# Performance work log

Hardware: AMD Instinct MI355X
Metric: run time of the kernel (lower is better)

The kernel has to match this reference:

```python
import jax, jax.numpy as jnp
import numpy as np

B, T, F, S, H, A = 32768, 64, 64, 5, 128, 16  # batch, obs_len, fut_len, state, hidden, adapter


def _gru_cell(x, h, Wih, Whh, bih, bhh):
    # PyTorch GRUCell math: gates ordered (r, z, n)
    gx = x @ Wih.T + bih
    gh = h @ Whh.T + bhh
    rx, zx, nx = jnp.split(gx, 3, axis=-1)
    rh, zh, nh = jnp.split(gh, 3, axis=-1)
    r = jax.nn.sigmoid(rx + rh)
    z = jax.nn.sigmoid(zx + zh)
    n = jnp.tanh(nx + r * nh)
    return (1.0 - z) * n + z * h


def setup_inputs() -> dict:
    key = jax.random.key(0)
    ks = jax.random.split(key, 24)
    p = lambda k, shp: jax.random.normal(k, shp, jnp.float32) * 0.05
    return {
        "obs": jax.random.normal(ks[0], (B, T, S), jnp.float32),
        "target": jax.random.normal(ks[1], (B, F, S), jnp.float32),
        "dataset_ids": jax.random.randint(ks[2], (B,), 0, 4),
        "enc_Wih": p(ks[3], (3 * H, S)), "enc_Whh": p(ks[4], (3 * H, H)),
        "enc_bih": p(ks[5], (3 * H,)), "enc_bhh": p(ks[6], (3 * H,)),
        "cell_Wih": p(ks[7], (3 * H, S)), "cell_Whh": p(ks[8], (3 * H, H)),
        "cell_bih": p(ks[9], (3 * H,)), "cell_bhh": p(ks[10], (3 * H,)),
        "head_W": p(ks[11], (S, H)), "head_b": p(ks[12], (S,)),
        "pp_W1": p(ks[13], (A, H)), "pp_b1": p(ks[14], (A,)),
        "pp_W2": p(ks[15], (H, A)), "pp_b2": p(ks[16], (H,)),
        "pk_W1": p(ks[17], (A, H)), "pk_b1": p(ks[18], (A,)),
        "pk_W2": p(ks[19], (H, A)), "pk_b2": p(ks[20], (H,)),
    }


def reference(obs, target, dataset_ids,
              enc_Wih, enc_Whh, enc_bih, enc_bhh,
              cell_Wih, cell_Whh, cell_bih, cell_bhh,
              head_W, head_b,
              pp_W1, pp_b1, pp_W2, pp_b2,
              pk_W1, pk_b1, pk_W2, pk_b2):
    b = obs.shape[0]
    # Encoder GRU over obs -> final hidden state [B, H]
    h0 = jnp.zeros((b, H), obs.dtype)
    def enc_step(h, x):
        return _gru_cell(x, h, enc_Wih, enc_Whh, enc_bih, enc_bhh), None
    h_t, _ = jax.lax.scan(enc_step, h0, jnp.swapaxes(obs, 0, 1))

    pm = (dataset_ids == 0)[:, None]  # pointodyssey routed to private_point
    km = (dataset_ids == 1)[:, None]  # kubric routed to private_kubric

    def adapt(h):
        dp = jax.nn.relu(h @ pp_W1.T + pp_b1) @ pp_W2.T + pp_b2
        dk = jax.nn.relu(h @ pk_W1.T + pk_b1) @ pk_W2.T + pk_b2
        return h + jnp.where(pm, dp, 0.0) + jnp.where(km, dk, 0.0)

    # Teacher-forced inputs: x_0 = obs[:, -1], x_t = target[:, t-1]
    xs = jnp.concatenate([obs[:, -1:, :], target[:, :-1, :]], axis=1)  # [B, F, S]
    def roll_step(h, x):
        h = _gru_cell(x, h, cell_Wih, cell_Whh, cell_bih, cell_bhh)
        h = adapt(h)
        return h, h @ head_W.T + head_b
    _, preds = jax.lax.scan(roll_step, h_t, jnp.swapaxes(xs, 0, 1))  # [F, B, S]
    return jnp.swapaxes(preds, 0, 1)  # [B, F, S]
```

## Files before the change

kernel.cpp:

```cpp
#include <hip/hip_runtime.h>

#define B_TOT 32768
#define T_OBS 64
#define F_FUT 64
#define S_DIM 5
#define H_DIM 128
#define A_DIM 16
#define R_BLK 64
#define NTHREADS 512
#define XSTR 320
#define HPAD 132
#define XPAD 36
#define APAD 24

typedef __attribute__((ext_vector_type(8))) short short8;
typedef __attribute__((ext_vector_type(4))) float f32x4;

union U8 { short8 v; unsigned int u[4]; unsigned short s[8]; };

__device__ __forceinline__ unsigned short f2bf(float f) {
  unsigned int u = __float_as_uint(f);
  u += 0x7FFFu + ((u >> 16) & 1u);
  return (unsigned short)(u >> 16);
}

__device__ __forceinline__ f32x4 MFMA(short8 a, short8 b, f32x4 c) {
  return __builtin_amdgcn_mfma_f32_16x16x32_bf16(a, b, c, 0, 0, 0);
}

__device__ __forceinline__ float sigm(float x) {
  return __builtin_amdgcn_rcpf(1.0f + __expf(-x));
}
__device__ __forceinline__ float tanh_(float x) {
  return 2.0f * __builtin_amdgcn_rcpf(1.0f + __expf(-2.0f * x)) - 1.0f;
}

__device__ __forceinline__ short8 load_w(const float* __restrict__ W, int ld,
                                         int g0, int gmax, int kmax, int ks,
                                         int lr, int lg) {
  U8 a;
  const int g = g0 + lr;
  #pragma unroll
  for (int i = 0; i < 8; ++i) {
    int k = 32 * ks + 16 * (i >> 2) + 4 * lg + (i & 3);
    float v = (g < gmax && k < kmax) ? W[g * ld + k] : 0.0f;
    a.s[i] = f2bf(v);
  }
  return a.v;
}

__device__ __forceinline__ void ld_bfrag(U8& b, const unsigned short* p) {
  uint2 t0 = *(const uint2*)p;
  uint2 t1 = *(const uint2*)(p + 16);
  b.u[0] = t0.x; b.u[1] = t0.y; b.u[2] = t1.x; b.u[3] = t1.y;
}

__device__ __forceinline__ void gru_step(
    const unsigned short* __restrict__ hb, const unsigned short* __restrict__ xb,
    const short8 (&fh)[3][4], const short8 (&fx)[3],
    const f32x4& brz0, const f32x4& brz1, const f32x4& bnh, const f32x4& bnx,
    const float (&h_old)[4][4], float (&hn)[4][4], int lr, int lg)
{
  f32x4 aR[4], aZ[4], aN[4], aX[4];
  #pragma unroll
  for (int rt = 0; rt < 4; ++rt) {
    const unsigned short* hp = hb + (rt * 16 + lr) * HPAD + 4 * lg;
    const unsigned short* xp = xb + (rt * 16 + lr) * XPAD + 4 * lg;
    U8 bx;
    { uint2 t = *(const uint2*)xp; bx.u[0] = t.x; bx.u[1] = t.y; bx.u[2] = 0u; bx.u[3] = 0u; }
    U8 bh0; ld_bfrag(bh0, hp);
    aR[rt] = MFMA(fh[0][0], bh0.v, brz0);
    aZ[rt] = MFMA(fh[1][0], bh0.v, brz1);
    aN[rt] = MFMA(fh[2][0], bh0.v, bnh);
    #pragma unroll
    for (int ks = 1; ks < 4; ++ks) {
      U8 bh; ld_bfrag(bh, hp + 32 * ks);
      aR[rt] = MFMA(fh[0][ks], bh.v, aR[rt]);
      aZ[rt] = MFMA(fh[1][ks], bh.v, aZ[rt]);
      aN[rt] = MFMA(fh[2][ks], bh.v, aN[rt]);
    }
    aR[rt] = MFMA(fx[0], bx.v, aR[rt]);
    aZ[rt] = MFMA(fx[1], bx.v, aZ[rt]);
    aX[rt] = MFMA(fx[2], bx.v, bnx);
  }
  #pragma unroll
  for (int rt = 0; rt < 4; ++rt) {
    #pragma unroll
    for (int i = 0; i < 4; ++i) {
      float r = sigm(aR[rt][i]);
      float z = sigm(aZ[rt][i]);
      float n = tanh_(aX[rt][i] + r * aN[rt][i]);
      hn[rt][i] = z * (h_old[rt][i] - n) + n;
    }
  }
}

__device__ __forceinline__ void write_h(unsigned short* hd, const float (&v)[4][4],
                                        int w, int lr, int lg) {
  #pragma unroll
  for (int rt = 0; rt < 4; ++rt) {
    uint2 t;
    t.x = (unsigned)f2bf(v[rt][0]) | ((unsigned)f2bf(v[rt][1]) << 16);
    t.y = (unsigned)f2bf(v[rt][2]) | ((unsigned)f2bf(v[rt][3]) << 16);
    *(uint2*)(hd + (rt * 16 + lr) * HPAD + 16 * w + 4 * lg) = t;
  }
}

__global__ __launch_bounds__(NTHREADS, 2) void trace_gru_kernel(
    const float* __restrict__ obs, const float* __restrict__ target,
    const int* __restrict__ ids,
    const float* __restrict__ eWih, const float* __restrict__ eWhh,
    const float* __restrict__ ebih, const float* __restrict__ ebhh,
    const float* __restrict__ cWih, const float* __restrict__ cWhh,
    const float* __restrict__ cbih, const float* __restrict__ cbhh,
    const float* __restrict__ headW, const float* __restrict__ headb,
    const float* __restrict__ ppW1, const float* __restrict__ ppb1,
    const float* __restrict__ ppW2, const float* __restrict__ ppb2,
    const float* __restrict__ pkW1, const float* __restrict__ pkb1,
    const float* __restrict__ pkW2, const float* __restrict__ pkb2,
    float* __restrict__ out)
{
  __shared__ __align__(16) unsigned short h_lds[2][R_BLK * HPAD];
  __shared__ __align__(16) unsigned short x_lds[2][R_BLK * XPAD];
  __shared__ __align__(16) unsigned short a_lds[2 * R_BLK * APAD];
  __shared__ __align__(16) unsigned short wd_lds[12 * 64 * 8];

  const int tid = threadIdx.x;
  const int lane = tid & 63;
  const int w = tid >> 6;
  const int lr = lane & 15;
  const int lg = lane >> 4;
  const int row0 = blockIdx.x * R_BLK;

  {
    unsigned int* p = (unsigned int*)&h_lds[0][0];
    for (int i = tid; i < R_BLK * HPAD / 2; i += NTHREADS) p[i] = 0u;
    unsigned int* q = (unsigned int*)&x_lds[0][0];
    for (int i = tid; i < 2 * R_BLK * XPAD / 2; i += NTHREADS) q[i] = 0u;
  }
  __syncthreads();

  const int sx_row = tid / 5;
  const int sx_s = tid - 5 * sx_row;
  if (tid < 320)
    x_lds[0][sx_row * XPAD + sx_s] = f2bf(obs[(row0 + sx_row) * XSTR + sx_s]);

  float pmf[4], kmf[4];
  #pragma unroll
  for (int rt = 0; rt < 4; ++rt) {
    int id = ids[row0 + rt * 16 + lr];
    pmf[rt] = (id == 0) ? 1.0f : 0.0f;
    kmf[rt] = (id == 1) ? 1.0f : 0.0f;
  }

  short8 fh[3][4], fx[3];
  f32x4 brz0, brz1, bnh, bnx;
  #pragma unroll
  for (int mt = 0; mt < 3; ++mt) {
    #pragma unroll
    for (int ks = 0; ks < 4; ++ks)
      fh[mt][ks] = load_w(eWhh, H_DIM, mt * H_DIM + 16 * w, 384, H_DIM, ks, lr, lg);
    fx[mt] = load_w(eWih, S_DIM, mt * H_DIM + 16 * w, 384, S_DIM, 0, lr, lg);
  }
  #pragma unroll
  for (int i = 0; i < 4; ++i) {
    int g = 16 * w + 4 * lg + i;
    brz0[i] = ebih[g] + ebhh[g];
    brz1[i] = ebih[H_DIM + g] + ebhh[H_DIM + g];
    bnh[i]  = ebhh[2 * H_DIM + g];
    bnx[i]  = ebih[2 * H_DIM + g];
  }

  float h_reg[4][4];
  #pragma unroll
  for (int rt = 0; rt < 4; ++rt)
    #pragma unroll
    for (int i = 0; i < 4; ++i) h_reg[rt][i] = 0.0f;

  __syncthreads();

  for (int u = 0; u < T_OBS; ++u) {
    float hn[4][4];
    gru_step(h_lds[u & 1], x_lds[u & 1], fh, fx, brz0, brz1, bnh, bnx, h_reg, hn, lr, lg);
    #pragma unroll
    for (int rt = 0; rt < 4; ++rt)
      #pragma unroll
      for (int i = 0; i < 4; ++i) h_reg[rt][i] = hn[rt][i];
    write_h(h_lds[(u + 1) & 1], h_reg, w, lr, lg);
    if (tid < 320) {
      int un = u + 1;
      int tsrc = (un < T_OBS) ? un : (T_OBS - 1);
      x_lds[un & 1][sx_row * XPAD + sx_s] =
          f2bf(obs[(row0 + sx_row) * XSTR + tsrc * S_DIM + sx_s]);
    }
    __syncthreads();
  }

  #pragma unroll
  for (int mt = 0; mt < 3; ++mt) {
    #pragma unroll
    for (int ks = 0; ks < 4; ++ks)
      fh[mt][ks] = load_w(cWhh, H_DIM, mt * H_DIM + 16 * w, 384, H_DIM, ks, lr, lg);
    fx[mt] = load_w(cWih, S_DIM, mt * H_DIM + 16 * w, 384, S_DIM, 0, lr, lg);
  }
  #pragma unroll
  for (int i = 0; i < 4; ++i) {
    int g = 16 * w + 4 * lg + i;
    brz0[i] = cbih[g] + cbhh[g];
    brz1[i] = cbih[H_DIM + g] + cbhh[H_DIM + g];
    bnh[i]  = cbhh[2 * H_DIM + g];
    bnx[i]  = cbih[2 * H_DIM + g];
  }
  short8 fW2[2];
  fW2[0] = load_w(ppW2, A_DIM, 16 * w, H_DIM, A_DIM, 0, lr, lg);
  fW2[1] = load_w(pkW2, A_DIM, 16 * w, H_DIM, A_DIM, 0, lr, lg);
  f32x4 b1v, b2v0, b2v1, hbv;
  {
    const float* b1p = (w & 1) ? pkb1 : ppb1;
    #pragma unroll
    for (int i = 0; i < 4; ++i) {
      b1v[i]  = b1p[4 * lg + i];
      b2v0[i] = ppb2[16 * w + 4 * lg + i];
      b2v1[i] = pkb2[16 * w + 4 * lg + i];
      int s = 4 * lg + i;
      hbv[i] = (s < S_DIM) ? headb[s] : 0.0f;
    }
  }
  for (int f = w; f < 12; f += 8) {
    short8 v;
    if (f < 8) {
      const float* W1 = (f >> 2) ? pkW1 : ppW1;
      v = load_w(W1, H_DIM, 0, A_DIM, H_DIM, f & 3, lr, lg);
    } else {
      v = load_w(headW, H_DIM, 0, S_DIM, H_DIM, f - 8, lr, lg);
    }
    *(short8*)&wd_lds[(f * 64 + lane) * 8] = v;
  }
  __syncthreads();

  for (int d = 0; d < F_FUT; ++d) {
    const int u = T_OBS + d;
    float hn[4][4];
    gru_step(h_lds[0], x_lds[u & 1], fh, fx, brz0, brz1, bnh, bnx, h_reg, hn, lr, lg);
    write_h(h_lds[1], hn, w, lr, lg);
    __syncthreads();

    {
      const int aa = w & 1, art = w >> 1;
      const unsigned short* hp = &h_lds[1][(art * 16 + lr) * HPAD + 4 * lg];
      U8 bh0; ld_bfrag(bh0, hp);
      f32x4 acc = MFMA(*(const short8*)&wd_lds[((aa * 4 + 0) * 64 + lane) * 8], bh0.v, b1v);
      #pragma unroll
      for (int ks = 1; ks < 4; ++ks) {
        U8 bh; ld_bfrag(bh, hp + 32 * ks);
        acc = MFMA(*(const short8*)&wd_lds[((aa * 4 + ks) * 64 + lane) * 8], bh.v, acc);
      }
      uint2 t;
      t.x = (unsigned)f2bf(fmaxf(acc[0], 0.f)) | ((unsigned)f2bf(fmaxf(acc[1], 0.f)) << 16);
      t.y = (unsigned)f2bf(fmaxf(acc[2], 0.f)) | ((unsigned)f2bf(fmaxf(acc[3], 0.f)) << 16);
      *(uint2*)&a_lds[(aa * R_BLK + art * 16 + lr) * APAD + 4 * lg] = t;
    }
    __syncthreads();

    #pragma unroll
    for (int rt = 0; rt < 4; ++rt) {
      U8 b0, b1_;
      { uint2 t = *(const uint2*)&a_lds[(0 * R_BLK + rt * 16 + lr) * APAD + 4 * lg];
        b0.u[0] = t.x; b0.u[1] = t.y; b0.u[2] = 0u; b0.u[3] = 0u; }
      { uint2 t = *(const uint2*)&a_lds[(1 * R_BLK + rt * 16 + lr) * APAD + 4 * lg];
        b1_.u[0] = t.x; b1_.u[1] = t.y; b1_.u[2] = 0u; b1_.u[3] = 0u; }
      f32x4 d0 = MFMA(fW2[0], b0.v, b2v0);
      f32x4 d1 = MFMA(fW2[1], b1_.v, b2v1);
      #pragma unroll
      for (int i = 0; i < 4; ++i)
        h_reg[rt][i] = hn[rt][i] + pmf[rt] * d0[i] + kmf[rt] * d1[i];
    }
    write_h(h_lds[0], h_reg, w, lr, lg);
    if (d < F_FUT - 1 && tid < 320) {
      int un = u + 1;
      x_lds[un & 1][sx_row * XPAD + sx_s] =
          f2bf(target[(row0 + sx_row) * XSTR + (un - T_OBS - 1) * S_DIM + sx_s]);
    }
    __syncthreads();

    if (w < 4) {
      const unsigned short* hp = &h_lds[0][(w * 16 + lr) * HPAD + 4 * lg];
      U8 bh0; ld_bfrag(bh0, hp);
      f32x4 acc = MFMA(*(const short8*)&wd_lds[((8 + 0) * 64 + lane) * 8], bh0.v, hbv);
      #pragma unroll
      for (int ks = 1; ks < 4; ++ks) {
        U8 bh; ld_bfrag(bh, hp + 32 * ks);
        acc = MFMA(*(const short8*)&wd_lds[((8 + ks) * 64 + lane) * 8], bh.v, acc);
      }
      float* op = out + (size_t)((row0 + w * 16 + lr) * F_FUT + d) * S_DIM;
      if (lg == 0) { op[0] = acc[0]; op[1] = acc[1]; op[2] = acc[2]; op[3] = acc[3]; }
      else if (lg == 1) { op[4] = acc[0]; }
    }
  }
}

extern "C" void kernel_launch(void* const* d_in, const int* in_sizes, int n_in,
                              void* d_out, int out_size, void* d_ws, size_t ws_size,
                              hipStream_t stream) {
  (void)in_sizes; (void)n_in; (void)out_size; (void)d_ws; (void)ws_size;
  const float* obs    = (const float*)d_in[0];
  const float* target = (const float*)d_in[1];
  const int*   ids    = (const int*)d_in[2];
  const float* eWih = (const float*)d_in[3];
  const float* eWhh = (const float*)d_in[4];
  const float* ebih = (const float*)d_in[5];
  const float* ebhh = (const float*)d_in[6];
  const float* cWih = (const float*)d_in[7];
  const float* cWhh = (const float*)d_in[8];
  const float* cbih = (const float*)d_in[9];
  const float* cbhh = (const float*)d_in[10];
  const float* headW = (const float*)d_in[11];
  const float* headb = (const float*)d_in[12];
  const float* ppW1 = (const float*)d_in[13];
  const float* ppb1 = (const float*)d_in[14];
  const float* ppW2 = (const float*)d_in[15];
  const float* ppb2 = (const float*)d_in[16];
  const float* pkW1 = (const float*)d_in[17];
  const float* pkb1 = (const float*)d_in[18];
  const float* pkW2 = (const float*)d_in[19];
  const float* pkb2 = (const float*)d_in[20];

  dim3 grid(B_TOT / R_BLK), block(NTHREADS);
  trace_gru_kernel<<<grid, block, 0, stream>>>(
      obs, target, ids,
      eWih, eWhh, ebih, ebhh,
      cWih, cWhh, cbih, cbhh,
      headW, headb,
      ppW1, ppb1, ppW2, ppb2,
      pkW1, pkb1, pkW2, pkb2,
      (float*)d_out);
}
```

Measured before the change: 793.4 us.

## Swizzle hidden-state LDS layout, prescale gate weights, prefetch inputs, fuse GRU epilogue

Replaces the padded hidden-state LDS layout with an XOR-style swizzled 128-wide layout. This allows single 16-byte reads per MFMA B fragment instead of two 8-byte reads. Gate weights and biases are prescaled by log2(e) so activations use exp2 directly, and bf16 packing uses the hardware v_cvt_pk_bf16_f32 instruction. Per-row-tile state writes are fused into the GRU step, and next-step inputs are prefetched from global memory a step ahead to hide load latency. The risks are bf16 rounding of prescaled weights and higher register pressure from the prefetch.

```diff
diff --git a/kernel.cpp b/kernel.cpp
--- a/kernel.cpp
+++ b/kernel.cpp
@@ -9,14 +9,23 @@
 #define R_BLK 64
 #define NTHREADS 512
 #define XSTR 320
-#define HPAD 132
+#define HSTR 128
 #define XPAD 36
 #define APAD 24
 
+#define LOG2E 1.4426950408889634f
+#define L2E2  2.8853900817779268f
+
 typedef __attribute__((ext_vector_type(8))) short short8;
 typedef __attribute__((ext_vector_type(4))) float f32x4;
 
 union U8 { short8 v; unsigned int u[4]; unsigned short s[8]; };
+
+#if __has_builtin(__builtin_amdgcn_exp2f)
+#define EXP2(x) __builtin_amdgcn_exp2f(x)
+#else
+#define EXP2(x) exp2f(x)
+#endif
 
 __device__ __forceinline__ unsigned short f2bf(float f) {
   unsigned int u = __float_as_uint(f);
@@ -24,85 +33,91 @@
   return (unsigned short)(u >> 16);
 }
 
+__device__ __forceinline__ unsigned cvtpk(float a, float b) {
+  unsigned r;
+  asm("v_cvt_pk_bf16_f32 %0, %1, %2" : "=v"(r) : "v"(a), "v"(b));
+  return r;
+}
+
 __device__ __forceinline__ f32x4 MFMA(short8 a, short8 b, f32x4 c) {
   return __builtin_amdgcn_mfma_f32_16x16x32_bf16(a, b, c, 0, 0, 0);
 }
 
-__device__ __forceinline__ float sigm(float x) {
-  return __builtin_amdgcn_rcpf(1.0f + __expf(-x));
-}
-__device__ __forceinline__ float tanh_(float x) {
-  return 2.0f * __builtin_amdgcn_rcpf(1.0f + __expf(-2.0f * x)) - 1.0f;
+__device__ __forceinline__ short8 h_read(const unsigned short* base, int row, int ks, int lg) {
+  return *(const short8*)(base + row * HSTR + (((4 * ks + lg + row) & 15) << 3));
+}
+__device__ __forceinline__ void h_write(unsigned short* base, int row, int w, int lg,
+                                        unsigned lo, unsigned hi) {
+  unsigned short* p = base + row * HSTR +
+                      (((4 * (w >> 1) + lg + row) & 15) << 3) + ((w & 1) << 2);
+  *(uint2*)p = make_uint2(lo, hi);
 }
 
 __device__ __forceinline__ short8 load_w(const float* __restrict__ W, int ld,
                                          int g0, int gmax, int kmax, int ks,
-                                         int lr, int lg) {
+                                         int lr, int lg, float scale) {
   U8 a;
   const int g = g0 + lr;
   #pragma unroll
   for (int i = 0; i < 8; ++i) {
     int k = 32 * ks + 16 * (i >> 2) + 4 * lg + (i & 3);
-    float v = (g < gmax && k < kmax) ? W[g * ld + k] : 0.0f;
+    float v = (g < gmax && k < kmax) ? W[g * ld + k] * scale : 0.0f;
     a.s[i] = f2bf(v);
   }
   return a.v;
 }
 
-__device__ __forceinline__ void ld_bfrag(U8& b, const unsigned short* p) {
-  uint2 t0 = *(const uint2*)p;
-  uint2 t1 = *(const uint2*)(p + 16);
-  b.u[0] = t0.x; b.u[1] = t0.y; b.u[2] = t1.x; b.u[3] = t1.y;
+__device__ __forceinline__ float xload(const float* __restrict__ obs,
+                                       const float* __restrict__ tgt,
+                                       int row, int s, int v) {
+  v = (v < 127) ? v : 127;
+  if (v < 65) {
+    int t = (v < 64) ? v : 63;
+    return obs[(size_t)row * XSTR + t * S_DIM + s];
+  }
+  return tgt[(size_t)row * XSTR + (v - 65) * S_DIM + s];
 }
 
 __device__ __forceinline__ void gru_step(
     const unsigned short* __restrict__ hb, const unsigned short* __restrict__ xb,
+    unsigned short* __restrict__ hd,
     const short8 (&fh)[3][4], const short8 (&fx)[3],
     const f32x4& brz0, const f32x4& brz1, const f32x4& bnh, const f32x4& bnx,
-    const float (&h_old)[4][4], float (&hn)[4][4], int lr, int lg)
+    float (&h_reg)[4][4], int w, int lr, int lg)
 {
-  f32x4 aR[4], aZ[4], aN[4], aX[4];
   #pragma unroll
   for (int rt = 0; rt < 4; ++rt) {
-    const unsigned short* hp = hb + (rt * 16 + lr) * HPAD + 4 * lg;
-    const unsigned short* xp = xb + (rt * 16 + lr) * XPAD + 4 * lg;
+    const int row = rt * 16 + lr;
     U8 bx;
-    { uint2 t = *(const uint2*)xp; bx.u[0] = t.x; bx.u[1] = t.y; bx.u[2] = 0u; bx.u[3] = 0u; }
-    U8 bh0; ld_bfrag(bh0, hp);
-    aR[rt] = MFMA(fh[0][0], bh0.v, brz0);
-    aZ[rt] = MFMA(fh[1][0], bh0.v, brz1);
-    aN[rt] = MFMA(fh[2][0], bh0.v, bnh);
+    { uint2 t = *(const uint2*)(xb + row * XPAD + 4 * lg);
+      bx.u[0] = t.x; bx.u[1] = t.y; bx.u[2] = 0u; bx.u[3] = 0u; }
+    short8 bh = h_read(hb, row, 0, lg);
+    f32x4 aR = MFMA(fh[0][0], bh, brz0);
+    f32x4 aZ = MFMA(fh[1][0], bh, brz1);
+    f32x4 aN = MFMA(fh[2][0], bh, bnh);
     #pragma unroll
     for (int ks = 1; ks < 4; ++ks) {
-      U8 bh; ld_bfrag(bh, hp + 32 * ks);
-      aR[rt] = MFMA(fh[0][ks], bh.v, aR[rt]);
-      aZ[rt] = MFMA(fh[1][ks], bh.v, aZ[rt]);
-      aN[rt] = MFMA(fh[2][ks], bh.v, aN[rt]);
-    }
-    aR[rt] = MFMA(fx[0], bx.v, aR[rt]);
-    aZ[rt] = MFMA(fx[1], bx.v, aZ[rt]);
-    aX[rt] = MFMA(fx[2], bx.v, bnx);
-  }
-  #pragma unroll
-  for (int rt = 0; rt < 4; ++rt) {
+      bh = h_read(hb, row, ks, lg);
+      aR = MFMA(fh[0][ks], bh, aR);
+      aZ = MFMA(fh[1][ks], bh, aZ);
+      aN = MFMA(fh[2][ks], bh, aN);
+    }
+    aR = MFMA(fx[0], bx.v, aR);
+    aZ = MFMA(fx[1], bx.v, aZ);
+    f32x4 aX = MFMA(fx[2], bx.v, bnx);
+    float hn0, hn1, hn2, hn3;
     #pragma unroll
     for (int i = 0; i < 4; ++i) {
-      float r = sigm(aR[rt][i]);
-      float z = sigm(aZ[rt][i]);
-      float n = tanh_(aX[rt][i] + r * aN[rt][i]);
-      hn[rt][i] = z * (h_old[rt][i] - n) + n;
-    }
-  }
-}
-
-__device__ __forceinline__ void write_h(unsigned short* hd, const float (&v)[4][4],
-                                        int w, int lr, int lg) {
-  #pragma unroll
-  for (int rt = 0; rt < 4; ++rt) {
-    uint2 t;
-    t.x = (unsigned)f2bf(v[rt][0]) | ((unsigned)f2bf(v[rt][1]) << 16);
-    t.y = (unsigned)f2bf(v[rt][2]) | ((unsigned)f2bf(v[rt][3]) << 16);
-    *(uint2*)(hd + (rt * 16 + lr) * HPAD + 16 * w + 4 * lg) = t;
+      float r = __builtin_amdgcn_rcpf(1.0f + EXP2(-aR[i]));
+      float z = __builtin_amdgcn_rcpf(1.0f + EXP2(-aZ[i]));
+      float v = fmaf(r, aN[i], aX[i]);
+      float q = __builtin_amdgcn_rcpf(1.0f + EXP2(-v));
+      float n = fmaf(2.0f, q, -1.0f);
+      float h = fmaf(z, h_reg[rt][i] - n, n);
+      h_reg[rt][i] = h;
+      if (i == 0) hn0 = h; else if (i == 1) hn1 = h; else if (i == 2) hn2 = h; else hn3 = h;
+    }
+    h_write(hd, row, w, lg, cvtpk(hn0, hn1), cvtpk(hn2, hn3));
   }
 }
 
@@ -120,7 +135,7 @@
     const float* __restrict__ pkW2, const float* __restrict__ pkb2,
     float* __restrict__ out)
 {
-  __shared__ __align__(16) unsigned short h_lds[2][R_BLK * HPAD];
+  __shared__ __align__(16) unsigned short h_lds[2][R_BLK * HSTR];
   __shared__ __align__(16) unsigned short x_lds[2][R_BLK * XPAD];
   __shared__ __align__(16) unsigned short a_lds[2 * R_BLK * APAD];
   __shared__ __align__(16) unsigned short wd_lds[12 * 64 * 8];
@@ -134,16 +149,20 @@
 
   {
     unsigned int* p = (unsigned int*)&h_lds[0][0];
-    for (int i = tid; i < R_BLK * HPAD / 2; i += NTHREADS) p[i] = 0u;
+    for (int i = tid; i < R_BLK * HSTR / 2; i += NTHREADS) p[i] = 0u;
     unsigned int* q = (unsigned int*)&x_lds[0][0];
     for (int i = tid; i < 2 * R_BLK * XPAD / 2; i += NTHREADS) q[i] = 0u;
   }
   __syncthreads();
 
+  const bool xa = (tid < 320);
   const int sx_row = tid / 5;
   const int sx_s = tid - 5 * sx_row;
-  if (tid < 320)
-    x_lds[0][sx_row * XPAD + sx_s] = f2bf(obs[(row0 + sx_row) * XSTR + sx_s]);
+  float xe = 0.f;
+  if (xa) {
+    x_lds[0][sx_row * XPAD + sx_s] = f2bf(xload(obs, target, row0 + sx_row, sx_s, 0));
+    xe = xload(obs, target, row0 + sx_row, sx_s, 1);
+  }
 
   float pmf[4], kmf[4];
   #pragma unroll
@@ -157,18 +176,19 @@
   f32x4 brz0, brz1, bnh, bnx;
   #pragma unroll
   for (int mt = 0; mt < 3; ++mt) {
+    const float sc = (mt == 2) ? L2E2 : LOG2E;
     #pragma unroll
     for (int ks = 0; ks < 4; ++ks)
-      fh[mt][ks] = load_w(eWhh, H_DIM, mt * H_DIM + 16 * w, 384, H_DIM, ks, lr, lg);
-    fx[mt] = load_w(eWih, S_DIM, mt * H_DIM + 16 * w, 384, S_DIM, 0, lr, lg);
+      fh[mt][ks] = load_w(eWhh, H_DIM, mt * H_DIM + 16 * w, 384, H_DIM, ks, lr, lg, sc);
+    fx[mt] = load_w(eWih, S_DIM, mt * H_DIM + 16 * w, 384, S_DIM, 0, lr, lg, sc);
   }
   #pragma unroll
   for (int i = 0; i < 4; ++i) {
     int g = 16 * w + 4 * lg + i;
-    brz0[i] = ebih[g] + ebhh[g];
-    brz1[i] = ebih[H_DIM + g] + ebhh[H_DIM + g];
-    bnh[i]  = ebhh[2 * H_DIM + g];
-    bnx[i]  = ebih[2 * H_DIM + g];
+    brz0[i] = (ebih[g] + ebhh[g]) * LOG2E;
+    brz1[i] = (ebih[H_DIM + g] + ebhh[H_DIM + g]) * LOG2E;
+    bnh[i]  = ebhh[2 * H_DIM + g] * L2E2;
+    bnx[i]  = ebih[2 * H_DIM + g] * L2E2;
   }
 
   float h_reg[4][4];
@@ -180,40 +200,34 @@
   __syncthreads();
 
   for (int u = 0; u < T_OBS; ++u) {
-    float hn[4][4];
-    gru_step(h_lds[u & 1], x_lds[u & 1], fh, fx, brz0, brz1, bnh, bnx, h_reg, hn, lr, lg);
-    #pragma unroll
-    for (int rt = 0; rt < 4; ++rt)
-      #pragma unroll
-      for (int i = 0; i < 4; ++i) h_reg[rt][i] = hn[rt][i];
-    write_h(h_lds[(u + 1) & 1], h_reg, w, lr, lg);
-    if (tid < 320) {
-      int un = u + 1;
-      int tsrc = (un < T_OBS) ? un : (T_OBS - 1);
-      x_lds[un & 1][sx_row * XPAD + sx_s] =
-          f2bf(obs[(row0 + sx_row) * XSTR + tsrc * S_DIM + sx_s]);
-    }
+    float xn = 0.f;
+    if (xa) xn = xload(obs, target, row0 + sx_row, sx_s, u + 2);
+    gru_step(&h_lds[u & 1][0], &x_lds[u & 1][0], &h_lds[(u + 1) & 1][0],
+             fh, fx, brz0, brz1, bnh, bnx, h_reg, w, lr, lg);
+    if (xa) x_lds[(u + 1) & 1][sx_row * XPAD + sx_s] = f2bf(xe);
     __syncthreads();
+    xe = xn;
   }
 
   #pragma unroll
   for (int mt = 0; mt < 3; ++mt) {
+    const float sc = (mt == 2) ? L2E2 : LOG2E;
     #pragma unroll
     for (int ks = 0; ks < 4; ++ks)
-      fh[mt][ks] = load_w(cWhh, H_DIM, mt * H_DIM + 16 * w, 384, H_DIM, ks, lr, lg);
-    fx[mt] = load_w(cWih, S_DIM, mt * H_DIM + 16 * w, 384, S_DIM, 0, lr, lg);
+      fh[mt][ks] = load_w(cWhh, H_DIM, mt * H_DIM + 16 * w, 384, H_DIM, ks, lr, lg, sc);
+    fx[mt] = load_w(cWih, S_DIM, mt * H_DIM + 16 * w, 384, S_DIM, 0, lr, lg, sc);
   }
   #pragma unroll
   for (int i = 0; i < 4; ++i) {
     int g = 16 * w + 4 * lg + i;
-    brz0[i] = cbih[g] + cbhh[g];
-    brz1[i] = cbih[H_DIM + g] + cbhh[H_DIM + g];
-    bnh[i]  = cbhh[2 * H_DIM + g];
-    bnx[i]  = cbih[2 * H_DIM + g];
+    brz0[i] = (cbih[g] + cbhh[g]) * LOG2E;
+    brz1[i] = (cbih[H_DIM + g] + cbhh[H_DIM + g]) * LOG2E;
+    bnh[i]  = cbhh[2 * H_DIM + g] * L2E2;
+    bnx[i]  = cbih[2 * H_DIM + g] * L2E2;
   }
   short8 fW2[2];
-  fW2[0] = load_w(ppW2, A_DIM, 16 * w, H_DIM, A_DIM, 0, lr, lg);
-  fW2[1] = load_w(pkW2, A_DIM, 16 * w, H_DIM, A_DIM, 0, lr, lg);
+  fW2[0] = load_w(ppW2, A_DIM, 16 * w, H_DIM, A_DIM, 0, lr, lg, 1.0f);
+  fW2[1] = load_w(pkW2, A_DIM, 16 * w, H_DIM, A_DIM, 0, lr, lg, 1.0f);
   f32x4 b1v, b2v0, b2v1, hbv;
   {
     const float* b1p = (w & 1) ? pkb1 : ppb1;
@@ -230,9 +244,9 @@
     short8 v;
     if (f < 8) {
       const float* W1 = (f >> 2) ? pkW1 : ppW1;
-      v = load_w(W1, H_DIM, 0, A_DIM, H_DIM, f & 3, lr, lg);
+      v = load_w(W1, H_DIM, 0, A_DIM, H_DIM, f & 3, lr, lg, 1.0f);
     } else {
-      v = load_w(headW, H_DIM, 0, S_DIM, H_DIM, f - 8, lr, lg);
+      v = load_w(headW, H_DIM, 0, S_DIM, H_DIM, f - 8, lr, lg, 1.0f);
     }
     *(short8*)&wd_lds[(f * 64 + lane) * 8] = v;
   }
@@ -240,62 +254,64 @@
 
   for (int d = 0; d < F_FUT; ++d) {
     const int u = T_OBS + d;
-    float hn[4][4];
-    gru_step(h_lds[0], x_lds[u & 1], fh, fx, brz0, brz1, bnh, bnx, h_reg, hn, lr, lg);
-    write_h(h_lds[1], hn, w, lr, lg);
+    float xn = 0.f;
+    if (xa) xn = xload(obs, target, row0 + sx_row, sx_s, u + 2);
+    gru_step(&h_lds[0][0], &x_lds[u & 1][0], &h_lds[1][0],
+             fh, fx, brz0, brz1, bnh, bnx, h_reg, w, lr, lg);
     __syncthreads();
 
     {
       const int aa = w & 1, art = w >> 1;
-      const unsigned short* hp = &h_lds[1][(art * 16 + lr) * HPAD + 4 * lg];
-      U8 bh0; ld_bfrag(bh0, hp);
-      f32x4 acc = MFMA(*(const short8*)&wd_lds[((aa * 4 + 0) * 64 + lane) * 8], bh0.v, b1v);
+      const int arow = art * 16 + lr;
+      short8 bh = h_read(&h_lds[1][0], arow, 0, lg);
+      f32x4 acc = MFMA(*(const short8*)&wd_lds[((aa * 4 + 0) * 64 + lane) * 8], bh, b1v);
       #pragma unroll
       for (int ks = 1; ks < 4; ++ks) {
-        U8 bh; ld_bfrag(bh, hp + 32 * ks);
-        acc = MFMA(*(const short8*)&wd_lds[((aa * 4 + ks) * 64 + lane) * 8], bh.v, acc);
+        bh = h_read(&h_lds[1][0], arow, ks, lg);
+        acc = MFMA(*(const short8*)&wd_lds[((aa * 4 + ks) * 64 + lane) * 8], bh, acc);
       }
-      uint2 t;
-      t.x = (unsigned)f2bf(fmaxf(acc[0], 0.f)) | ((unsigned)f2bf(fmaxf(acc[1], 0.f)) << 16);
-      t.y = (unsigned)f2bf(fmaxf(acc[2], 0.f)) | ((unsigned)f2bf(fmaxf(acc[3], 0.f)) << 16);
-      *(uint2*)&a_lds[(aa * R_BLK + art * 16 + lr) * APAD + 4 * lg] = t;
+      unsigned lo = cvtpk(fmaxf(acc[0], 0.f), fmaxf(acc[1], 0.f));
+      unsigned hi = cvtpk(fmaxf(acc[2], 0.f), fmaxf(acc[3], 0.f));
+      *(uint2*)&a_lds[(aa * R_BLK + arow) * APAD + 4 * lg] = make_uint2(lo, hi);
     }
     __syncthreads();
 
     #pragma unroll
     for (int rt = 0; rt < 4; ++rt) {
+      const int arow = rt * 16 + lr;
       U8 b0, b1_;
-      { uint2 t = *(const uint2*)&a_lds[(0 * R_BLK + rt * 16 + lr) * APAD + 4 * lg];
+      { uint2 t = *(const uint2*)&a_lds[(0 * R_BLK + arow) * APAD + 4 * lg];
         b0.u[0] = t.x; b0.u[1] = t.y; b0.u[2] = 0u; b0.u[3] = 0u; }
-      { uint2 t = *(const uint2*)&a_lds[(1 * R_BLK + rt * 16 + lr) * APAD + 4 * lg];
+      { uint2 t = *(const uint2*)&a_lds[(1 * R_BLK + arow) * APAD + 4 * lg];
         b1_.u[0] = t.x; b1_.u[1] = t.y; b1_.u[2] = 0u; b1_.u[3] = 0u; }
       f32x4 d0 = MFMA(fW2[0], b0.v, b2v0);
       f32x4 d1 = MFMA(fW2[1], b1_.v, b2v1);
+      float hv0, hv1, hv2, hv3;
       #pragma unroll
-      for (int i = 0; i < 4; ++i)
-        h_reg[rt][i] = hn[rt][i] + pmf[rt] * d0[i] + kmf[rt] * d1[i];
-    }
-    write_h(h_lds[0], h_reg, w, lr, lg);
-    if (d < F_FUT - 1 && tid < 320) {
-      int un = u + 1;
-      x_lds[un & 1][sx_row * XPAD + sx_s] =
-          f2bf(target[(row0 + sx_row) * XSTR + (un - T_OBS - 1) * S_DIM + sx_s]);
-    }
+      for (int i = 0; i < 4; ++i) {
+        float h = h_reg[rt][i] + pmf[rt] * d0[i] + kmf[rt] * d1[i];
+        h_reg[rt][i] = h;
+        if (i == 0) hv0 = h; else if (i == 1) hv1 = h; else if (i == 2) hv2 = h; else hv3 = h;
+      }
+      h_write(&h_lds[0][0], arow, w, lg, cvtpk(hv0, hv1), cvtpk(hv2, hv3));
+    }
+    if (xa) x_lds[(u + 1) & 1][sx_row * XPAD + sx_s] = f2bf(xe);
     __syncthreads();
 
     if (w < 4) {
-      const unsigned short* hp = &h_lds[0][(w * 16 + lr) * HPAD + 4 * lg];
-      U8 bh0; ld_bfrag(bh0, hp);
-      f32x4 acc = MFMA(*(const short8*)&wd_lds[((8 + 0) * 64 + lane) * 8], bh0.v, hbv);
+      const int arow = w * 16 + lr;
+      short8 bh = h_read(&h_lds[0][0], arow, 0, lg);
+      f32x4 acc = MFMA(*(const short8*)&wd_lds[((8 + 0) * 64 + lane) * 8], bh, hbv);
       #pragma unroll
       for (int ks = 1; ks < 4; ++ks) {
-        U8 bh; ld_bfrag(bh, hp + 32 * ks);
-        acc = MFMA(*(const short8*)&wd_lds[((8 + ks) * 64 + lane) * 8], bh.v, acc);
+        bh = h_read(&h_lds[0][0], arow, ks, lg);
+        acc = MFMA(*(const short8*)&wd_lds[((8 + ks) * 64 + lane) * 8], bh, acc);
       }
-      float* op = out + (size_t)((row0 + w * 16 + lr) * F_FUT + d) * S_DIM;
+      float* op = out + (size_t)((row0 + arow) * F_FUT + d) * S_DIM;
       if (lg == 0) { op[0] = acc[0]; op[1] = acc[1]; op[2] = acc[2]; op[3] = acc[3]; }
       else if (lg == 1) { op[4] = acc[0]; }
     }
+    xe = xn;
   }
 }
 
```

Measured after the change: 668.5 us. 15.7% less time.
